# Performance work log

Hardware: AMD Instinct MI355X
Metric: run time of the kernel (lower is better)

The kernel has to match this reference:

```python
import jax, jax.numpy as jnp
import numpy as np

N_P, N_A, D_MP = 200000, 100000, 64   # paper nodes, author nodes, metapath embed dim
E = 1200000                            # nnz per adjacency op
F_P, F_A = 256, 128                    # raw feature dims


def _spmm(row, col, val, z, n_out):
    # Sparse [n_out, n_in] @ dense [n_in, d]: out[i] = sum_{e: row[e]==i} val[e] * z[col[e]]
    return jax.ops.segment_sum(val[:, None] * z[col], row, num_segments=n_out)


def setup_inputs() -> dict:
    key = jax.random.key(0)
    k = jax.random.split(key, 10)
    return {
        "x_paper": jax.random.normal(k[0], (N_P, F_P), jnp.float32),
        "x_author": jax.random.normal(k[1], (N_A, F_A), jnp.float32),
        "W_paper": jax.random.normal(k[2], (F_P, D_MP), jnp.float32) / np.float32(np.sqrt(F_P)),
        "W_author": jax.random.normal(k[3], (F_A, D_MP), jnp.float32) / np.float32(np.sqrt(F_A)),
        "pa_row": jax.random.randint(k[4], (E,), 0, N_A, jnp.int32),
        "pa_col": jax.random.randint(k[5], (E,), 0, N_P, jnp.int32),
        "pa_val": jax.random.uniform(k[6], (E,), jnp.float32),
        "ap_row": jax.random.randint(k[7], (E,), 0, N_P, jnp.int32),
        "ap_col": jax.random.randint(k[8], (E,), 0, N_A, jnp.int32),
        "ap_val": jax.random.uniform(k[9], (E,), jnp.float32),
    }


def reference(x_paper, x_author, W_paper, W_author,
              pa_row, pa_col, pa_val, ap_row, ap_col, ap_val):
    # per-node-type projection (nn.Linear, no bias)
    zp = x_paper @ W_paper    # [N_P, D_MP]
    za = x_author @ W_author  # [N_A, D_MP]

    # metapath P-A-P: ops = [pa (N_A x N_P), ap (N_P x N_A)]
    h = _spmm(pa_row, pa_col, pa_val, zp, N_A)
    pap = _spmm(ap_row, ap_col, ap_val, h, N_P)

    # metapath P-A-P-A-P: 4 chained SpMMs
    h2 = _spmm(pa_row, pa_col, pa_val, pap, N_A)
    papap = _spmm(ap_row, ap_col, ap_val, h2, N_P)

    # metapath A-P-A: ops = [ap (N_P x N_A), pa (N_A x N_P)]
    g = _spmm(ap_row, ap_col, ap_val, za, N_P)
    apa = _spmm(pa_row, pa_col, pa_val, g, N_A)

    return (pap, papap, apa)
```

## Files before the change

### kernel.cpp

```cpp
#include <hip/hip_runtime.h>
#include <hip/hip_fp16.h>

#define NP 200000
#define NA 100000
#define NE 1200000
#define NTOT (NA + NP)
#define NBP_GEMM 3125
#define NBA_GEMM 1563

typedef _Float16 half8 __attribute__((ext_vector_type(8)));
typedef float f32x4 __attribute__((ext_vector_type(4)));


__global__ __launch_bounds__(256) void hist2_k(const int* __restrict__ pa_row, const int* __restrict__ ap_row,
                                               int* __restrict__ cnt_all) {
    int i = blockIdx.x * blockDim.x + threadIdx.x;
    int stride = gridDim.x * blockDim.x;
    for (; i < 2 * NE; i += stride) {
        if (i < NE) atomicAdd(&cnt_all[pa_row[i]], 1);
        else        atomicAdd(&cnt_all[NA + ap_row[i - NE]], 1);
    }
}

__global__ __launch_bounds__(256) void scan1_k(const int* __restrict__ in, int* __restrict__ out,
                                               int* __restrict__ bsums, int n) {
    __shared__ int lds[256];
    int t = threadIdx.x;
    int base = blockIdx.x * 1024 + t * 4;
    int v0 = (base + 0 < n) ? in[base + 0] : 0;
    int v1 = (base + 1 < n) ? in[base + 1] : 0;
    int v2 = (base + 2 < n) ? in[base + 2] : 0;
    int v3 = (base + 3 < n) ? in[base + 3] : 0;
    lds[t] = v0 + v1 + v2 + v3;
    __syncthreads();
    for (int off = 1; off < 256; off <<= 1) {
        int x = (t >= off) ? lds[t - off] : 0;
        __syncthreads();
        lds[t] += x;
        __syncthreads();
    }
    if (t == 255) bsums[blockIdx.x] = lds[255];
    int run = (t == 0) ? 0 : lds[t - 1];
    if (base + 0 < n) out[base + 0] = run; run += v0;
    if (base + 1 < n) out[base + 1] = run; run += v1;
    if (base + 2 < n) out[base + 2] = run; run += v2;
    if (base + 3 < n) out[base + 3] = run;
}

__global__ void scan2_k(int* bsums, int nb) {
    __shared__ int lds[512];
    int t = threadIdx.x;
    int v = (t < nb) ? bsums[t] : 0;
    lds[t] = v;
    __syncthreads();
    for (int off = 1; off < 512; off <<= 1) {
        int x = (t >= off) ? lds[t - off] : 0;
        __syncthreads();
        lds[t] += x;
        __syncthreads();
    }
    if (t < nb) bsums[t] = lds[t] - v;
}

__global__ __launch_bounds__(256) void scan3_k(int* __restrict__ out, const int* __restrict__ bsums, int n) {
    int add = bsums[blockIdx.x];
    int base = blockIdx.x * 1024 + threadIdx.x * 4;
#pragma unroll
    for (int j = 0; j < 4; j++)
        if (base + j < n) out[base + j] += add;
}

__global__ __launch_bounds__(256) void scatter2_k(const int* __restrict__ pa_row, const int* __restrict__ pa_col,
                                                  const float* __restrict__ pa_val,
                                                  const int* __restrict__ ap_row, const int* __restrict__ ap_col,
                                                  const float* __restrict__ ap_val,
                                                  const int* __restrict__ off_all, int* __restrict__ cursor,
                                                  int2* __restrict__ csr_all) {
    int i = blockIdx.x * blockDim.x + threadIdx.x;
    int stride = gridDim.x * blockDim.x;
    for (; i < 2 * NE; i += stride) {
        if (i < NE) {
            int r = pa_row[i];
            int pos = off_all[r] + atomicAdd(&cursor[r], 1);
            csr_all[pos] = make_int2(pa_col[i], __float_as_int(pa_val[i]));
        } else {
            int r = NA + ap_row[i - NE];
            int pos = off_all[r] + atomicAdd(&cursor[r], 1);
            csr_all[pos] = make_int2(ap_col[i - NE], __float_as_int(ap_val[i - NE]));
        }
    }
}


__device__ __forceinline__ void fma_h8(float acc[8], float v, uint4 r) {
    __half2 h0 = *(__half2*)&r.x;
    __half2 h1 = *(__half2*)&r.y;
    __half2 h2 = *(__half2*)&r.z;
    __half2 h3 = *(__half2*)&r.w;
    float2 f0 = __half22float2(h0);
    float2 f1 = __half22float2(h1);
    float2 f2 = __half22float2(h2);
    float2 f3 = __half22float2(h3);
    acc[0] = fmaf(v, f0.x, acc[0]);
    acc[1] = fmaf(v, f0.y, acc[1]);
    acc[2] = fmaf(v, f1.x, acc[2]);
    acc[3] = fmaf(v, f1.y, acc[3]);
    acc[4] = fmaf(v, f2.x, acc[4]);
    acc[5] = fmaf(v, f2.y, acc[5]);
    acc[6] = fmaf(v, f3.x, acc[6]);
    acc[7] = fmaf(v, f3.y, acc[7]);
}

__device__ __forceinline__ void store_h8(uint4* out16, int g, int l, const float acc[8]) {
    __half2 p0 = __floats2half2_rn(acc[0], acc[1]);
    __half2 p1 = __floats2half2_rn(acc[2], acc[3]);
    __half2 p2 = __floats2half2_rn(acc[4], acc[5]);
    __half2 p3 = __floats2half2_rn(acc[6], acc[7]);
    uint4 o;
    o.x = *(unsigned*)&p0;
    o.y = *(unsigned*)&p1;
    o.z = *(unsigned*)&p2;
    o.w = *(unsigned*)&p3;
    out16[(size_t)g * 8 + l] = o;
}

__device__ __forceinline__ void store_f8(float4* out32, int g, int l, const float acc[8]) {
    out32[(size_t)g * 16 + l * 2 + 0] = make_float4(acc[0], acc[1], acc[2], acc[3]);
    out32[(size_t)g * 16 + l * 2 + 1] = make_float4(acc[4], acc[5], acc[6], acc[7]);
}

__global__ __launch_bounds__(256) void spmm_k(const int2* __restrict__ csr, const int* __restrict__ off,
                                              const int* __restrict__ cnt, const uint4* __restrict__ z,
                                              float4* __restrict__ out32, uint4* __restrict__ out16,
                                              int nrows) {
    int g = blockIdx.x * 32 + (threadIdx.x >> 3);
    int l = threadIdx.x & 7;
    if (g >= nrows) return;
    int start = off[g], deg = cnt[g];
    float acc[8];
#pragma unroll
    for (int i = 0; i < 8; i++) acc[i] = 0.f;

    if (deg > 0) {
        int2 e[8];
#pragma unroll
        for (int k = 0; k < 8; k++) e[k] = csr[start + min(k, deg - 1)];
        for (int j = 0; j < deg; j += 8) {
            uint4 r[8];
#pragma unroll
            for (int k = 0; k < 8; k++) r[k] = z[e[k].x * 8 + l];
            float v[8];
#pragma unroll
            for (int k = 0; k < 8; k++) v[k] = (j + k < deg) ? __int_as_float(e[k].y) : 0.f;
            int2 en[8];
            bool more = (j + 8) < deg;
            if (more) {
#pragma unroll
                for (int k = 0; k < 8; k++) en[k] = csr[start + min(j + 8 + k, deg - 1)];
            }
#pragma unroll
            for (int k = 0; k < 8; k++) fma_h8(acc, v[k], r[k]);
            if (more) {
#pragma unroll
                for (int k = 0; k < 8; k++) e[k] = en[k];
            }
        }
    }
    if (out32) store_f8(out32, g, l, acc);
    if (out16) store_h8(out16, g, l, acc);
}

__global__ __launch_bounds__(256) void spmm2_k(const int2* __restrict__ csr, const int* __restrict__ off,
                                               const int* __restrict__ cnt,
                                               const uint4* __restrict__ zA, const uint4* __restrict__ zB,
                                               float4* __restrict__ outA32, uint4* __restrict__ outA16,
                                               float4* __restrict__ outB32, uint4* __restrict__ outB16,
                                               int nrows) {
    int g = blockIdx.x * 32 + (threadIdx.x >> 3);
    int l = threadIdx.x & 7;
    if (g >= nrows) return;
    int start = off[g], deg = cnt[g];
    float accA[8], accB[8];
#pragma unroll
    for (int i = 0; i < 8; i++) { accA[i] = 0.f; accB[i] = 0.f; }

    if (deg > 0) {
        int2 e[8];
#pragma unroll
        for (int k = 0; k < 8; k++) e[k] = csr[start + min(k, deg - 1)];
        for (int j = 0; j < deg; j += 8) {
            uint4 rA[8], rB[8];
#pragma unroll
            for (int k = 0; k < 8; k++) {
                int idx = e[k].x * 8 + l;
                rA[k] = zA[idx];
                rB[k] = zB[idx];
            }
            float v[8];
#pragma unroll
            for (int k = 0; k < 8; k++) v[k] = (j + k < deg) ? __int_as_float(e[k].y) : 0.f;
            int2 en[8];
            bool more = (j + 8) < deg;
            if (more) {
#pragma unroll
                for (int k = 0; k < 8; k++) en[k] = csr[start + min(j + 8 + k, deg - 1)];
            }
#pragma unroll
            for (int k = 0; k < 8; k++) {
                fma_h8(accA, v[k], rA[k]);
                fma_h8(accB, v[k], rB[k]);
            }
            if (more) {
#pragma unroll
                for (int k = 0; k < 8; k++) e[k] = en[k];
            }
        }
    }
    if (outA32) store_f8(outA32, g, l, accA);
    if (outA16) store_h8(outA16, g, l, accA);
    if (outB32) store_f8(outB32, g, l, accB);
    if (outB16) store_h8(outB16, g, l, accB);
}


__global__ __launch_bounds__(256) void wconv_k(const float* __restrict__ Wp, const float* __restrict__ Wa,
                                               __half* __restrict__ wtP, __half* __restrict__ wtA) {
    int i = blockIdx.x * 256 + threadIdx.x;
    int stride = gridDim.x * 256;
    for (int idx = i; idx < 64 * 256; idx += stride) {
        int c = idx >> 8, k = idx & 255;
        wtP[idx] = (__half)Wp[k * 64 + c];
    }
    for (int idx = i; idx < 64 * 128; idx += stride) {
        int c = idx >> 7, k = idx & 127;
        wtA[idx] = (__half)Wa[k * 64 + c];
    }
}

__global__ __launch_bounds__(256) void gemm_mfma_k(const float* __restrict__ xP, const float* __restrict__ xA,
                                                   const __half* __restrict__ wtP, const __half* __restrict__ wtA,
                                                   __half* __restrict__ zP, __half* __restrict__ zA) {
    int b = blockIdx.x;
    const float* x;
    const __half* wt;
    __half* z;
    int K, nrows, r0;
    if (b < NBP_GEMM) { x = xP; wt = wtP; z = zP; K = 256; nrows = NP; r0 = b * 64; }
    else              { x = xA; wt = wtA; z = zA; K = 128; nrows = NA; r0 = (b - NBP_GEMM) * 64; }

    int w = threadIdx.x >> 6;
    int l = threadIdx.x & 63;
    int arow = r0 + w * 16 + (l & 15);
    int kq = (l >> 4) * 8;

    f32x4 acc0 = {0.f, 0.f, 0.f, 0.f};
    f32x4 acc1 = {0.f, 0.f, 0.f, 0.f};
    f32x4 acc2 = {0.f, 0.f, 0.f, 0.f};
    f32x4 acc3 = {0.f, 0.f, 0.f, 0.f};

    for (int k0 = 0; k0 < K; k0 += 32) {
        half8 a;
        if (arow < nrows) {
            const float* xp = x + (size_t)arow * K + k0 + kq;
            float4 f0 = *(const float4*)xp;
            float4 f1 = *(const float4*)(xp + 4);
            a[0] = (_Float16)f0.x; a[1] = (_Float16)f0.y;
            a[2] = (_Float16)f0.z; a[3] = (_Float16)f0.w;
            a[4] = (_Float16)f1.x; a[5] = (_Float16)f1.y;
            a[6] = (_Float16)f1.z; a[7] = (_Float16)f1.w;
        } else {
#pragma unroll
            for (int j = 0; j < 8; j++) a[j] = (_Float16)0.f;
        }
        const __half* wbase = wt + (size_t)(l & 15) * K + k0 + kq;
        half8 b0 = *(const half8*)(wbase);
        half8 b1 = *(const half8*)(wbase + (size_t)16 * K);
        half8 b2 = *(const half8*)(wbase + (size_t)32 * K);
        half8 b3 = *(const half8*)(wbase + (size_t)48 * K);
        acc0 = __builtin_amdgcn_mfma_f32_16x16x32_f16(a, b0, acc0, 0, 0, 0);
        acc1 = __builtin_amdgcn_mfma_f32_16x16x32_f16(a, b1, acc1, 0, 0, 0);
        acc2 = __builtin_amdgcn_mfma_f32_16x16x32_f16(a, b2, acc2, 0, 0, 0);
        acc3 = __builtin_amdgcn_mfma_f32_16x16x32_f16(a, b3, acc3, 0, 0, 0);
    }

    int orow0 = r0 + w * 16 + (l >> 4) * 4;
    int col = l & 15;
#pragma unroll
    for (int i = 0; i < 4; i++) {
        int r = orow0 + i;
        if (r < nrows) {
            __half* zr = z + (size_t)r * 64;
            zr[col +  0] = (__half)acc0[i];
            zr[col + 16] = (__half)acc1[i];
            zr[col + 32] = (__half)acc2[i];
            zr[col + 48] = (__half)acc3[i];
        }
    }
}


extern "C" void kernel_launch(void* const* d_in, const int* in_sizes, int n_in,
                              void* d_out, int out_size, void* d_ws, size_t ws_size,
                              hipStream_t stream) {
    const float* x_paper  = (const float*)d_in[0];
    const float* x_author = (const float*)d_in[1];
    const float* W_paper  = (const float*)d_in[2];
    const float* W_author = (const float*)d_in[3];
    const int*   pa_row   = (const int*)d_in[4];
    const int*   pa_col   = (const int*)d_in[5];
    const float* pa_val   = (const float*)d_in[6];
    const int*   ap_row   = (const int*)d_in[7];
    const int*   ap_col   = (const int*)d_in[8];
    const float* ap_val   = (const float*)d_in[9];

    char* ws = (char*)d_ws;
    size_t o = 0;
    auto alloc = [&](size_t bytes) -> char* {
        char* p = ws + o;
        o += (bytes + 255) & ~(size_t)255;
        return p;
    };
    __half* zp16  = (__half*)alloc((size_t)NP * 64 * 2);
    __half* za16  = (__half*)alloc((size_t)NA * 64 * 2);
    __half* h16   = (__half*)alloc((size_t)NA * 64 * 2);
    __half* pap16 = (__half*)alloc((size_t)NP * 64 * 2);
    int2*  csr_all = (int2*)alloc((size_t)2 * NE * 8);
    int* cnt_all = (int*)alloc(NTOT * 4);
    int* off_all = (int*)alloc(NTOT * 4);
    int* cursor  = (int*)alloc(NTOT * 4);
    int* bsums   = (int*)alloc(1024 * 4);
    __half* wtP  = (__half*)alloc(64 * 256 * 2);
    __half* wtA  = (__half*)alloc(64 * 128 * 2);

    float* out_pap   = (float*)d_out;
    float* out_papap = out_pap + (size_t)NP * 64;
    float* out_apa   = out_papap + (size_t)NP * 64;

    const int nb_tot = (NTOT + 1023) / 1024;

    hipMemsetAsync(cnt_all, 0, NTOT * 4, stream);
    hist2_k<<<1024, 256, 0, stream>>>(pa_row, ap_row, cnt_all);
    scan1_k<<<nb_tot, 256, 0, stream>>>(cnt_all, off_all, bsums, NTOT);
    scan2_k<<<1, 512, 0, stream>>>(bsums, nb_tot);
    scan3_k<<<nb_tot, 256, 0, stream>>>(off_all, bsums, NTOT);
    hipMemsetAsync(cursor, 0, NTOT * 4, stream);
    scatter2_k<<<1024, 256, 0, stream>>>(pa_row, pa_col, pa_val, ap_row, ap_col, ap_val,
                                         off_all, cursor, csr_all);

    wconv_k<<<64, 256, 0, stream>>>(W_paper, W_author, wtP, wtA);
    gemm_mfma_k<<<NBP_GEMM + NBA_GEMM, 256, 0, stream>>>(x_paper, x_author, wtP, wtA, zp16, za16);

    const int* off_pa = off_all;
    const int* cnt_pa = cnt_all;
    const int* off_ap = off_all + NA;
    const int* cnt_ap = cnt_all + NA;

    spmm_k<<<NA / 32, 256, 0, stream>>>(csr_all, off_pa, cnt_pa, (const uint4*)zp16,
                                        nullptr, (uint4*)h16, NA);
    spmm2_k<<<NP / 32, 256, 0, stream>>>(csr_all, off_ap, cnt_ap,
                                         (const uint4*)h16, (const uint4*)za16,
                                         (float4*)out_pap, (uint4*)pap16,
                                         nullptr, (uint4*)zp16, NP);
    spmm2_k<<<NA / 32, 256, 0, stream>>>(csr_all, off_pa, cnt_pa,
                                         (const uint4*)pap16, (const uint4*)zp16,
                                         nullptr, (uint4*)h16,
                                         (float4*)out_apa, nullptr, NA);
    spmm_k<<<NP / 32, 256, 0, stream>>>(csr_all, off_ap, cnt_ap, (const uint4*)h16,
                                        (float4*)out_papap, nullptr, NP);
}
```

Baseline: 784.3 us.

## Replace global-atomic COO-to-CSR build with two-pass bucketed partition

Replaces the histogram and scatter, which used global atomics per edge, with a bucketed radix-style partition. First, per-chunk LDS histograms over 1024-row buckets are scanned into offsets and edges are staged by bucket. Then per-bucket kernels count rows and place edges using LDS atomics only. This aims to remove contended global atomics and random scattered writes, at the cost of an extra staging buffer, more kernel launches, and only 294 blocks in the per-bucket passes.

```diff
diff --git a/kernel.cpp b/kernel.cpp
--- a/kernel.cpp
+++ b/kernel.cpp
@@ -8,19 +8,16 @@
 #define NBP_GEMM 3125
 #define NBA_GEMM 1563
 
+#define CHUNK 4096
+#define NCHUNK 586
+#define NBUCKA 98
+#define NBUCKP 196
+#define NBUCK (NBUCKA + NBUCKP)
+#define MATN (NBUCK * NCHUNK)
+
 typedef _Float16 half8 __attribute__((ext_vector_type(8)));
 typedef float f32x4 __attribute__((ext_vector_type(4)));
 
-
-__global__ __launch_bounds__(256) void hist2_k(const int* __restrict__ pa_row, const int* __restrict__ ap_row,
-                                               int* __restrict__ cnt_all) {
-    int i = blockIdx.x * blockDim.x + threadIdx.x;
-    int stride = gridDim.x * blockDim.x;
-    for (; i < 2 * NE; i += stride) {
-        if (i < NE) atomicAdd(&cnt_all[pa_row[i]], 1);
-        else        atomicAdd(&cnt_all[NA + ap_row[i - NE]], 1);
-    }
-}
 
 __global__ __launch_bounds__(256) void scan1_k(const int* __restrict__ in, int* __restrict__ out,
                                                int* __restrict__ bsums, int n) {
@@ -47,13 +44,13 @@
     if (base + 3 < n) out[base + 3] = run;
 }
 
-__global__ void scan2_k(int* bsums, int nb) {
-    __shared__ int lds[512];
+__global__ __launch_bounds__(1024) void scan2_k(int* bsums, int nb) {
+    __shared__ int lds[1024];
     int t = threadIdx.x;
     int v = (t < nb) ? bsums[t] : 0;
     lds[t] = v;
     __syncthreads();
-    for (int off = 1; off < 512; off <<= 1) {
+    for (int off = 1; off < 1024; off <<= 1) {
         int x = (t >= off) ? lds[t - off] : 0;
         __syncthreads();
         lds[t] += x;
@@ -70,24 +67,89 @@
         if (base + j < n) out[base + j] += add;
 }
 
-__global__ __launch_bounds__(256) void scatter2_k(const int* __restrict__ pa_row, const int* __restrict__ pa_col,
-                                                  const float* __restrict__ pa_val,
-                                                  const int* __restrict__ ap_row, const int* __restrict__ ap_col,
-                                                  const float* __restrict__ ap_val,
-                                                  const int* __restrict__ off_all, int* __restrict__ cursor,
-                                                  int2* __restrict__ csr_all) {
-    int i = blockIdx.x * blockDim.x + threadIdx.x;
-    int stride = gridDim.x * blockDim.x;
-    for (; i < 2 * NE; i += stride) {
-        if (i < NE) {
-            int r = pa_row[i];
-            int pos = off_all[r] + atomicAdd(&cursor[r], 1);
-            csr_all[pos] = make_int2(pa_col[i], __float_as_int(pa_val[i]));
-        } else {
-            int r = NA + ap_row[i - NE];
-            int pos = off_all[r] + atomicAdd(&cursor[r], 1);
-            csr_all[pos] = make_int2(ap_col[i - NE], __float_as_int(ap_val[i - NE]));
-        }
+
+__device__ __forceinline__ int bucket_gbase(int b) {
+    return (b < NBUCKA) ? (b << 10) : NA + ((b - NBUCKA) << 10);
+}
+__device__ __forceinline__ int bucket_nrows(int b) {
+    return (b < NBUCKA) ? min(1024, NA - (b << 10)) : min(1024, NP - ((b - NBUCKA) << 10));
+}
+
+__global__ __launch_bounds__(256) void part_cnt_k(const int* __restrict__ pa_row, const int* __restrict__ ap_row,
+                                                  int* __restrict__ mat) {
+    __shared__ int lh[NBUCK];
+    int t = threadIdx.x, c = blockIdx.x;
+    for (int b = t; b < NBUCK; b += 256) lh[b] = 0;
+    __syncthreads();
+    int base = c * CHUNK;
+#pragma unroll
+    for (int k = 0; k < CHUNK / 256; k++) {
+        int i = base + k * 256 + t;
+        if (i < 2 * NE) {
+            int b = (i < NE) ? (pa_row[i] >> 10) : (NBUCKA + (ap_row[i - NE] >> 10));
+            atomicAdd(&lh[b], 1);
+        }
+    }
+    __syncthreads();
+    for (int b = t; b < NBUCK; b += 256) mat[b * NCHUNK + c] = lh[b];
+}
+
+__global__ __launch_bounds__(256) void part_scat_k(const int* __restrict__ pa_row, const int* __restrict__ pa_col,
+                                                   const float* __restrict__ pa_val,
+                                                   const int* __restrict__ ap_row, const int* __restrict__ ap_col,
+                                                   const float* __restrict__ ap_val,
+                                                   const int* __restrict__ matoff, int2* __restrict__ staged) {
+    __shared__ int lc[NBUCK];
+    int t = threadIdx.x, c = blockIdx.x;
+    for (int b = t; b < NBUCK; b += 256) lc[b] = 0;
+    __syncthreads();
+    int base = c * CHUNK;
+#pragma unroll
+    for (int k = 0; k < CHUNK / 256; k++) {
+        int i = base + k * 256 + t;
+        if (i < 2 * NE) {
+            int b, rl, col; float v;
+            if (i < NE) {
+                int r = pa_row[i];
+                b = r >> 10; rl = r & 1023; col = pa_col[i]; v = pa_val[i];
+            } else {
+                int r = ap_row[i - NE];
+                b = NBUCKA + (r >> 10); rl = r & 1023; col = ap_col[i - NE]; v = ap_val[i - NE];
+            }
+            int rk = atomicAdd(&lc[b], 1);
+            staged[matoff[b * NCHUNK + c] + rk] = make_int2((rl << 20) | col, __float_as_int(v));
+        }
+    }
+}
+
+__global__ __launch_bounds__(256) void bcnt_k(const int2* __restrict__ staged, const int* __restrict__ matoff,
+                                              int* __restrict__ cnt_all) {
+    __shared__ int lcnt[1024];
+    int t = threadIdx.x, b = blockIdx.x;
+    for (int r = t; r < 1024; r += 256) lcnt[r] = 0;
+    __syncthreads();
+    int s = matoff[b * NCHUNK];
+    int e = (b + 1 < NBUCK) ? matoff[(b + 1) * NCHUNK] : 2 * NE;
+    for (int i = s + t; i < e; i += 256) atomicAdd(&lcnt[staged[i].x >> 20], 1);
+    __syncthreads();
+    int gb = bucket_gbase(b), nr = bucket_nrows(b);
+    for (int r = t; r < nr; r += 256) cnt_all[gb + r] = lcnt[r];
+}
+
+__global__ __launch_bounds__(256) void place_k(const int2* __restrict__ staged, const int* __restrict__ matoff,
+                                               const int* __restrict__ off_all, int2* __restrict__ csr_all) {
+    __shared__ int lcur[1024];
+    int t = threadIdx.x, b = blockIdx.x;
+    for (int r = t; r < 1024; r += 256) lcur[r] = 0;
+    __syncthreads();
+    int s = matoff[b * NCHUNK];
+    int e = (b + 1 < NBUCK) ? matoff[(b + 1) * NCHUNK] : 2 * NE;
+    int gb = bucket_gbase(b);
+    for (int i = s + t; i < e; i += 256) {
+        int2 rec = staged[i];
+        int rl = rec.x >> 20;
+        int pos = off_all[gb + rl] + atomicAdd(&lcur[rl], 1);
+        csr_all[pos] = make_int2(rec.x & 0xFFFFF, rec.y);
     }
 }
 
@@ -325,9 +387,11 @@
     __half* h16   = (__half*)alloc((size_t)NA * 64 * 2);
     __half* pap16 = (__half*)alloc((size_t)NP * 64 * 2);
     int2*  csr_all = (int2*)alloc((size_t)2 * NE * 8);
+    int2*  staged  = (int2*)alloc((size_t)2 * NE * 8);
+    int* mat     = (int*)alloc((size_t)MATN * 4);
+    int* matoff  = (int*)alloc((size_t)MATN * 4);
     int* cnt_all = (int*)alloc(NTOT * 4);
     int* off_all = (int*)alloc(NTOT * 4);
-    int* cursor  = (int*)alloc(NTOT * 4);
     int* bsums   = (int*)alloc(1024 * 4);
     __half* wtP  = (__half*)alloc(64 * 256 * 2);
     __half* wtA  = (__half*)alloc(64 * 128 * 2);
@@ -336,16 +400,20 @@
     float* out_papap = out_pap + (size_t)NP * 64;
     float* out_apa   = out_papap + (size_t)NP * 64;
 
+    const int nb_mat = (MATN + 1023) / 1024;
     const int nb_tot = (NTOT + 1023) / 1024;
 
-    hipMemsetAsync(cnt_all, 0, NTOT * 4, stream);
-    hist2_k<<<1024, 256, 0, stream>>>(pa_row, ap_row, cnt_all);
+    part_cnt_k<<<NCHUNK, 256, 0, stream>>>(pa_row, ap_row, mat);
+    scan1_k<<<nb_mat, 256, 0, stream>>>(mat, matoff, bsums, MATN);
+    scan2_k<<<1, 1024, 0, stream>>>(bsums, nb_mat);
+    scan3_k<<<nb_mat, 256, 0, stream>>>(matoff, bsums, MATN);
+    part_scat_k<<<NCHUNK, 256, 0, stream>>>(pa_row, pa_col, pa_val, ap_row, ap_col, ap_val,
+                                            matoff, staged);
+    bcnt_k<<<NBUCK, 256, 0, stream>>>(staged, matoff, cnt_all);
     scan1_k<<<nb_tot, 256, 0, stream>>>(cnt_all, off_all, bsums, NTOT);
-    scan2_k<<<1, 512, 0, stream>>>(bsums, nb_tot);
+    scan2_k<<<1, 1024, 0, stream>>>(bsums, nb_tot);
     scan3_k<<<nb_tot, 256, 0, stream>>>(off_all, bsums, NTOT);
-    hipMemsetAsync(cursor, 0, NTOT * 4, stream);
-    scatter2_k<<<1024, 256, 0, stream>>>(pa_row, pa_col, pa_val, ap_row, ap_col, ap_val,
-                                         off_all, cursor, csr_all);
+    place_k<<<NBUCK, 256, 0, stream>>>(staged, matoff, off_all, csr_all);
 
     wconv_k<<<64, 256, 0, stream>>>(W_paper, W_author, wtP, wtA);
     gemm_mfma_k<<<NBP_GEMM + NBA_GEMM, 256, 0, stream>>>(x_paper, x_author, wtP, wtA, zp16, za16);
```

New measurement: 678.2 us. 13.5% less time.
